# Optimization experiments

Measured on AMD Instinct MI355X. Metric: run time of the kernel, lower is better.

The kernel has to match this reference:

```python
import jax, jax.numpy as jnp
import numpy as np

NUM_EMBEDDINGS = 2048
EMBEDDING_DIM = 512
COMMITMENT_COST = 0.25


def setup_inputs() -> dict:
    key = jax.random.key(0)
    k1, k2 = jax.random.split(key)
    IP_score = jax.random.normal(k1, (256, 51, 512), dtype=jnp.float32)
    emb_weight = jax.random.normal(k2, (NUM_EMBEDDINGS, EMBEDDING_DIM), dtype=jnp.float32)
    return {"IP_score": IP_score, "emb_weight": emb_weight}


def reference(IP_score, emb_weight):
    sg = jax.lax.stop_gradient
    bs, kpts, seq = IP_score.shape
    x = IP_score.reshape(bs, kpts // 3, 3, seq)          # [bs, kpts/3, 3, D]
    flat = x.reshape(-1, seq)                             # [N, D], N = bs*kpts

    # pairwise squared L2 distances to codebook: [N, K]
    d = (jnp.sum(flat * flat, axis=1, keepdims=True)
         + jnp.sum(emb_weight * emb_weight, axis=1)
         - 2.0 * flat @ emb_weight.T)

    # nearest (argmin) and the 3rd-smallest index (coding_idx[:, 2] in torch)
    _, idx3 = jax.lax.top_k(-d, 3)                        # ascending distance order
    nearest = idx3[:, 0]
    third = idx3[:, 2]

    quantized = jnp.take(emb_weight, nearest, axis=0).reshape(x.shape)
    second_quantized = jnp.take(emb_weight, third, axis=0).reshape(x.shape)

    # commitment loss (quantized is detached in the original)
    e_latent_loss = jnp.mean((sg(quantized) - x) ** 2)
    k_loss = COMMITMENT_COST * e_latent_loss

    # straight-through estimator
    quantized_st = x + sg(quantized - x)
    second_st = x + sg(second_quantized - x)

    feature_EMA = quantized_st.reshape(bs, kpts, seq)
    sec_EMA = second_st.reshape(bs, kpts, seq)

    cp_score = 1.0 - (jnp.linalg.norm(feature_EMA - IP_score)
                      / jnp.linalg.norm(sec_EMA - IP_score))
    return (cp_score, k_loss, feature_EMA)
```

## Files before the change

kernel.cpp:

```cpp
#include <hip/hip_runtime.h>
#include <hip/hip_bf16.h>
#include <math.h>

#define RM 13056
#define KD 512
#define NE 2048
#define NELEM 6684672.0

#define BM 128
#define BN 256
#define BK 32
#define NKT (KD / BK)
#define NBLK (NE / BN)
#define NCAND (NBLK * 4)
#define NTAIL (RM / 4)

typedef __attribute__((ext_vector_type(8))) short bf16x8;
typedef __attribute__((ext_vector_type(4))) float f32x4;
typedef unsigned long long ull;

__device__ __forceinline__ void dma16(const void* g, void* l) {
  __builtin_amdgcn_global_load_lds((const __attribute__((address_space(1))) void*)g,
                                   (__attribute__((address_space(3))) void*)l, 16, 0, 0);
}

__device__ __forceinline__ ull packdi(float d, int ix) {
  unsigned u = __float_as_uint(d);
  u ^= (unsigned)((int)u >> 31) | 0x80000000u;
  return ((ull)u << 32) | (unsigned)ix;
}

#define XB (RM * 64 / 256)
#define EB (NE * 64 / 256)
#define NB (NE / 4)
__device__ __forceinline__ void split_chunks(const float* __restrict__ src,
                                             unsigned short* __restrict__ hi,
                                             int rows, int o) {
  int t4 = o >> 2;
  int kt = t4 / rows;
  int row = t4 - kt * rows;
  int slot = o & 3;
  int q = slot ^ ((row >> 1) & 3);
  const float* s = src + (size_t)row * KD + kt * 32 + q * 8;
  float4 v0 = ((const float4*)s)[0];
  float4 v1 = ((const float4*)s)[1];
  float f[8] = {v0.x, v0.y, v0.z, v0.w, v1.x, v1.y, v1.z, v1.w};
  unsigned hh[4];
#pragma unroll
  for (int j = 0; j < 4; ++j) {
    __hip_bfloat16 b0 = __float2bfloat16(f[2 * j]);
    __hip_bfloat16 b1 = __float2bfloat16(f[2 * j + 1]);
    hh[j] = (unsigned)*(unsigned short*)&b0 | ((unsigned)*(unsigned short*)&b1 << 16);
  }
  ((uint4*)hi)[o] = make_uint4(hh[0], hh[1], hh[2], hh[3]);
}

__global__ __launch_bounds__(256) void k_prep(const float* __restrict__ X,
                                              const float* __restrict__ E,
                                              unsigned short* __restrict__ Xh,
                                              unsigned short* __restrict__ Eh,
                                              float* __restrict__ EN) {
  const int b = blockIdx.x, tid = threadIdx.x;
  if (b < XB) {
    split_chunks(X, Xh, RM, b * 256 + tid);
  } else if (b < XB + EB) {
    split_chunks(E, Eh, NE, (b - XB) * 256 + tid);
  } else {
    int n = (b - XB - EB) * 4 + (tid >> 6);
    int lane = tid & 63;
    const float* e = E + (size_t)n * KD;
    float s = 0.f;
#pragma unroll
    for (int j = 0; j < 8; ++j) { float v = e[lane + 64 * j]; s += v * v; }
#pragma unroll
    for (int off = 32; off; off >>= 1) s += __shfl_down(s, off);
    if (lane == 0) EN[n] = s;
  }
}

__device__ __forceinline__ int chidx(int row, int q) {
  return (row * 4 + (q ^ ((row >> 1) & 3))) * 8;
}

__global__ __launch_bounds__(256, 2) void k_dist_bf16(
    const unsigned short* __restrict__ Xh,
    const unsigned short* __restrict__ Eh,
    const float* __restrict__ EN, ull* __restrict__ cand) {
  __shared__ __align__(16) unsigned short sXh[2][BM * BK];
  __shared__ __align__(16) unsigned short sEh[2][BN * BK];
  __shared__ float sEN[BN];

  const int tid = threadIdx.x;
  const int lane = tid & 63;
  const int w = tid >> 6;
  const int quad = lane >> 4;
  const int lx = lane & 15;
  const int rowBase = blockIdx.x * BM;
  const int colBase = blockIdx.y * BN;

  sEN[tid] = EN[colBase + tid];

  int aidx[2], bidx[16];
#pragma unroll
  for (int mt = 0; mt < 2; ++mt) aidx[mt] = chidx(w * 32 + mt * 16 + lx, quad);
#pragma unroll
  for (int ct = 0; ct < 16; ++ct) bidx[ct] = chidx(ct * 16 + lx, quad);

  f32x4 acc[2][16];
#pragma unroll
  for (int mt = 0; mt < 2; ++mt)
#pragma unroll
    for (int ct = 0; ct < 16; ++ct) acc[mt][ct] = (f32x4){0.f, 0.f, 0.f, 0.f};

  for (int kt2 = 0; kt2 < NKT / 2; ++kt2) {
    __syncthreads();
#pragma unroll
    for (int h = 0; h < 2; ++h) {
      const int kt = kt2 * 2 + h;
      const size_t xbase = ((size_t)kt * RM + rowBase) * 4;
      const size_t ebase = ((size_t)kt * NE + colBase) * 4;
#pragma unroll
      for (int i = 0; i < 2; ++i) {
        const int c = i * 256 + tid;
        const int ldsOff = (i * 256 + w * 64) * 8;
        dma16(Xh + (xbase + c) * 8, &sXh[h][ldsOff]);
      }
#pragma unroll
      for (int i = 0; i < 4; ++i) {
        const int c = i * 256 + tid;
        const int ldsOff = (i * 256 + w * 64) * 8;
        dma16(Eh + (ebase + c) * 8, &sEh[h][ldsOff]);
      }
    }
    __syncthreads();

#pragma unroll
    for (int h = 0; h < 2; ++h) {
      bf16x8 Ah[2];
#pragma unroll
      for (int mt = 0; mt < 2; ++mt) Ah[mt] = *(const bf16x8*)&sXh[h][aidx[mt]];
#pragma unroll
      for (int ct = 0; ct < 16; ++ct) {
        bf16x8 Bh = *(const bf16x8*)&sEh[h][bidx[ct]];
#pragma unroll
        for (int mt = 0; mt < 2; ++mt)
          acc[mt][ct] = __builtin_amdgcn_mfma_f32_16x16x32_bf16(Ah[mt], Bh, acc[mt][ct], 0, 0, 0);
      }
    }
  }

  float en[16];
#pragma unroll
  for (int ct = 0; ct < 16; ++ct) en[ct] = sEN[ct * 16 + lx];

#pragma unroll
  for (int mt = 0; mt < 2; ++mt) {
#pragma unroll
    for (int j = 0; j < 4; ++j) {
      float a0 = 3.4e38f, a1 = 3.4e38f, a2 = 3.4e38f, a3 = 3.4e38f;
      int i0 = 0x7fffffff, i1 = i0, i2 = i0, i3 = i0;
#pragma unroll
      for (int ct = 0; ct < 16; ++ct) {
        float d = en[ct] - 2.0f * acc[mt][ct][j];
        int ix = colBase + ct * 16 + lx;
        if (d < a3) {
          if (d < a2) { a3 = a2; i3 = i2;
            if (d < a1) { a2 = a1; i2 = i1;
              if (d < a0) { a1 = a0; i1 = i0; a0 = d; i0 = ix; }
              else { a1 = d; i1 = ix; } }
            else { a2 = d; i2 = ix; } }
          else { a3 = d; i3 = ix; }
        }
      }
      ull k0 = packdi(a0, i0), k1 = packdi(a1, i1);
      ull k2 = packdi(a2, i2), k3 = packdi(a3, i3);
      int pos = 0;
      ull res[4];
#pragma unroll
      for (int r = 0; r < 4; ++r) {
        ull h = pos == 0 ? k0 : pos == 1 ? k1 : pos == 2 ? k2 : pos == 3 ? k3 : ~0ull;
        ull m = h;
#pragma unroll
        for (int step = 1; step < 16; step <<= 1) {
          ull o = __shfl_xor(m, step, 16);
          m = o < m ? o : m;
        }
        res[r] = m;
        pos += (h == m) ? 1 : 0;
      }
      if (lx == 0) {
        int row = rowBase + w * 32 + mt * 16 + quad * 4 + j;
        ull* dst = cand + (size_t)row * NCAND + blockIdx.y * 4;
        dst[0] = res[0]; dst[1] = res[1]; dst[2] = res[2]; dst[3] = res[3];
      }
    }
  }
}

__device__ __forceinline__ void refine_core(const float* __restrict__ X,
                                            const float* __restrict__ E,
                                            const int* ci, int row,
                                            float* __restrict__ outF,
                                            double* __restrict__ part) {
  const int w = threadIdx.x >> 6, lane = threadIdx.x & 63;
  __shared__ double bs1[4], bs3[4];
  const float* xr = X + (size_t)row * KD;
  float4 x0 = *(const float4*)(xr + lane * 8);
  float4 x1 = *(const float4*)(xr + lane * 8 + 4);
  double a[8];
#pragma unroll
  for (int c = 0; c < 8; ++c) {
    const float* er = E + (size_t)ci[c] * KD;
    float4 e0 = *(const float4*)(er + lane * 8);
    float4 e1 = *(const float4*)(er + lane * 8 + 4);
    double s = 0.0;
    double d0 = (double)e0.x - (double)x0.x; s += d0 * d0;
    double d1 = (double)e0.y - (double)x0.y; s += d1 * d1;
    double d2 = (double)e0.z - (double)x0.z; s += d2 * d2;
    double d3 = (double)e0.w - (double)x0.w; s += d3 * d3;
    double d4 = (double)e1.x - (double)x1.x; s += d4 * d4;
    double d5 = (double)e1.y - (double)x1.y; s += d5 * d5;
    double d6 = (double)e1.z - (double)x1.z; s += d6 * d6;
    double d7 = (double)e1.w - (double)x1.w; s += d7 * d7;
    a[c] = s;
  }
#pragma unroll
  for (int c = 0; c < 8; ++c)
#pragma unroll
    for (int off = 32; off; off >>= 1) a[c] += __shfl_down(a[c], off);
  int best = 0;
  if (lane == 0) {
    double d[8]; int id[8];
#pragma unroll
    for (int c = 0; c < 8; ++c) { d[c] = a[c]; id[c] = ci[c]; }
    for (int i = 0; i < 8; ++i)
      for (int j = i + 1; j < 8; ++j)
        if (d[j] < d[i] || (d[j] == d[i] && id[j] < id[i])) {
          double dt = d[i]; d[i] = d[j]; d[j] = dt;
          int it = id[i]; id[i] = id[j]; id[j] = it;
        }
    bs1[w] = d[0];
    bs3[w] = d[2];
    best = id[0];
  }
  best = __shfl(best, 0);
  const float* er = E + (size_t)best * KD;
  *(float4*)(outF + (size_t)row * KD + lane * 8) = *(const float4*)(er + lane * 8);
  *(float4*)(outF + (size_t)row * KD + lane * 8 + 4) = *(const float4*)(er + lane * 8 + 4);
  __syncthreads();
  if (threadIdx.x == 0) {
    part[blockIdx.x * 2] = bs1[0] + bs1[1] + bs1[2] + bs1[3];
    part[blockIdx.x * 2 + 1] = bs3[0] + bs3[1] + bs3[2] + bs3[3];
  }
}

__device__ __forceinline__ ull sort64(ull k, int lane) {
#pragma unroll
  for (int kk = 2; kk <= 64; kk <<= 1) {
#pragma unroll
    for (int j = kk >> 1; j > 0; j >>= 1) {
      ull o = __shfl_xor(k, j, 64);
      bool dirUp = (lane & kk) == 0;
      bool lower = (lane & j) == 0;
      bool pl = o < k;
      bool take = (dirUp == lower) ? pl : !pl;
      if (take) k = o;
    }
  }
  return k;
}

__global__ __launch_bounds__(256) void k_mrf(const float* __restrict__ X,
                                             const float* __restrict__ E,
                                             const ull* __restrict__ cand,
                                             float* __restrict__ outF,
                                             double* __restrict__ part) {
  const int lane = threadIdx.x & 63;
  const int row = blockIdx.x * 4 + (threadIdx.x >> 6);
  ull k = lane < NCAND ? cand[(size_t)row * NCAND + lane] : ~0ull;
  k = sort64(k, lane);
  int ci[8];
#pragma unroll
  for (int c = 0; c < 8; ++c) ci[c] = (int)(__shfl(k, c, 64) & 0xffffffffull);
  refine_core(X, E, ci, row, outF, part);
}

__global__ __launch_bounds__(256) void k_fin(const double* __restrict__ part,
                                             float* __restrict__ out) {
  const int tid = threadIdx.x;
  double a1 = 0.0, a3 = 0.0;
  for (int r = tid; r < NTAIL; r += 256) { a1 += part[2 * r]; a3 += part[2 * r + 1]; }
#pragma unroll
  for (int off = 32; off; off >>= 1) {
    a1 += __shfl_down(a1, off);
    a3 += __shfl_down(a3, off);
  }
  __shared__ double s1[4], s3[4];
  const int w = tid >> 6, lane = tid & 63;
  if (lane == 0) { s1[w] = a1; s3[w] = a3; }
  __syncthreads();
  if (tid == 0) {
    double S1 = s1[0] + s1[1] + s1[2] + s1[3];
    double S3 = s3[0] + s3[1] + s3[2] + s3[3];
    out[0] = (float)(1.0 - sqrt(S1 / S3));
    out[1] = (float)(0.25 * S1 / NELEM);
  }
}

__global__ __launch_bounds__(256) void k_merge(const ull* __restrict__ cand,
                                               int* __restrict__ top8) {
  const int lane = threadIdx.x & 63;
  const int row = blockIdx.x * 4 + (threadIdx.x >> 6);
  ull k = lane < NCAND ? cand[(size_t)row * NCAND + lane] : ~0ull;
  k = sort64(k, lane);
  if (lane < 8) top8[(size_t)row * 8 + lane] = (int)(k & 0xffffffffull);
}

__global__ __launch_bounds__(256) void k_refine_fb(const float* __restrict__ X,
                                                   const float* __restrict__ E,
                                                   const int* __restrict__ top8,
                                                   float* __restrict__ outF,
                                                   double* __restrict__ part) {
  const int row = blockIdx.x * 4 + (threadIdx.x >> 6);
  int ci[8];
#pragma unroll
  for (int c = 0; c < 8; ++c) ci[c] = top8[(size_t)row * 8 + c];
  refine_core(X, E, ci, row, outF, part);
}

extern "C" void kernel_launch(void* const* d_in, const int* in_sizes, int n_in,
                              void* d_out, int out_size, void* d_ws, size_t ws_size,
                              hipStream_t stream) {
  const float* IP = (const float*)d_in[0];
  const float* EMB = (const float*)d_in[1];
  float* out = (float*)d_out;

  char* ws = (char*)d_ws;
  size_t off = 0;
  float* EN = (float*)(ws + off);        off += NE * 4;
  double* part = (double*)(ws + off);    off += (size_t)NTAIL * 2 * 8;
  int* top8 = (int*)(ws + off);          off += (size_t)RM * 8 * 4;
  unsigned short* Xh = (unsigned short*)(ws + off); off += (size_t)RM * KD * 2;
  unsigned short* Ehs = (unsigned short*)(ws + off); off += (size_t)NE * KD * 2;
  ull* candWs = (ull*)(ws + off);        off += (size_t)RM * NCAND * 8;
  const bool fused = ws_size >= off;

  ull* cand = fused ? candWs : (ull*)(out + 2);

  hipLaunchKernelGGL(k_prep, dim3(XB + EB + NB), dim3(256), 0, stream,
                     IP, EMB, Xh, Ehs, EN);
  hipLaunchKernelGGL(k_dist_bf16, dim3(RM / BM, NBLK), dim3(256), 0, stream,
                     Xh, Ehs, EN, cand);
  if (fused) {
    hipLaunchKernelGGL(k_mrf, dim3(NTAIL), dim3(256), 0, stream,
                       IP, EMB, cand, out + 2, part);
  } else {
    hipLaunchKernelGGL(k_merge, dim3(NTAIL), dim3(256), 0, stream, cand, top8);
    hipLaunchKernelGGL(k_refine_fb, dim3(NTAIL), dim3(256), 0, stream,
                       IP, EMB, top8, out + 2, part);
  }
  hipLaunchKernelGGL(k_fin, dim3(1), dim3(256), 0, stream, part, out);
}
```

Baseline: 179.8 us.

## Load bf16 MFMA operands directly from global memory, dropping LDS staging

Removes the LDS double-buffer staging (global_load_lds DMA plus barriers) from the distance GEMM kernel. Each lane now loads its A and B fragments straight from the pre-swizzled global layout into registers every k-step. This cuts the barriers and LDS traffic, but it loses reuse of B tiles across the four waves and of A tiles across the column tiles. The result is more redundant global/L2 reads and register pressure from 16 B vectors held in flight with no prefetch.

Result: slower. 218.7 us (+21.6%).

```diff
diff --git a/kernel.cpp b/kernel.cpp
--- a/kernel.cpp
+++ b/kernel.cpp
@@ -18,11 +18,6 @@
 typedef __attribute__((ext_vector_type(8))) short bf16x8;
 typedef __attribute__((ext_vector_type(4))) float f32x4;
 typedef unsigned long long ull;
-
-__device__ __forceinline__ void dma16(const void* g, void* l) {
-  __builtin_amdgcn_global_load_lds((const __attribute__((address_space(1))) void*)g,
-                                   (__attribute__((address_space(3))) void*)l, 16, 0, 0);
-}
 
 __device__ __forceinline__ ull packdi(float d, int ix) {
   unsigned u = __float_as_uint(d);
@@ -78,16 +73,10 @@
   }
 }
 
-__device__ __forceinline__ int chidx(int row, int q) {
-  return (row * 4 + (q ^ ((row >> 1) & 3))) * 8;
-}
-
 __global__ __launch_bounds__(256, 2) void k_dist_bf16(
     const unsigned short* __restrict__ Xh,
     const unsigned short* __restrict__ Eh,
     const float* __restrict__ EN, ull* __restrict__ cand) {
-  __shared__ __align__(16) unsigned short sXh[2][BM * BK];
-  __shared__ __align__(16) unsigned short sEh[2][BN * BK];
   __shared__ float sEN[BN];
 
   const int tid = threadIdx.x;
@@ -100,11 +89,18 @@
 
   sEN[tid] = EN[colBase + tid];
 
-  int aidx[2], bidx[16];
-#pragma unroll
-  for (int mt = 0; mt < 2; ++mt) aidx[mt] = chidx(w * 32 + mt * 16 + lx, quad);
-#pragma unroll
-  for (int ct = 0; ct < 16; ++ct) bidx[ct] = chidx(ct * 16 + lx, quad);
+  unsigned aoff[2];
+#pragma unroll
+  for (int mt = 0; mt < 2; ++mt) {
+    int row = rowBase + w * 32 + mt * 16 + lx;
+    aoff[mt] = (unsigned)((row * 4 + (quad ^ ((row >> 1) & 3))) * 16);
+  }
+  unsigned boff[16];
+#pragma unroll
+  for (int ct = 0; ct < 16; ++ct) {
+    int n = colBase + ct * 16 + lx;
+    boff[ct] = (unsigned)((n * 4 + (quad ^ ((n >> 1) & 3))) * 16);
+  }
 
   f32x4 acc[2][16];
 #pragma unroll
@@ -112,42 +108,25 @@
 #pragma unroll
     for (int ct = 0; ct < 16; ++ct) acc[mt][ct] = (f32x4){0.f, 0.f, 0.f, 0.f};
 
-  for (int kt2 = 0; kt2 < NKT / 2; ++kt2) {
-    __syncthreads();
-#pragma unroll
-    for (int h = 0; h < 2; ++h) {
-      const int kt = kt2 * 2 + h;
-      const size_t xbase = ((size_t)kt * RM + rowBase) * 4;
-      const size_t ebase = ((size_t)kt * NE + colBase) * 4;
-#pragma unroll
-      for (int i = 0; i < 2; ++i) {
-        const int c = i * 256 + tid;
-        const int ldsOff = (i * 256 + w * 64) * 8;
-        dma16(Xh + (xbase + c) * 8, &sXh[h][ldsOff]);
-      }
-#pragma unroll
-      for (int i = 0; i < 4; ++i) {
-        const int c = i * 256 + tid;
-        const int ldsOff = (i * 256 + w * 64) * 8;
-        dma16(Eh + (ebase + c) * 8, &sEh[h][ldsOff]);
-      }
+  const char* Xp = (const char*)Xh;
+  const char* Ep = (const char*)Eh;
+#pragma unroll 1
+  for (int kt = 0; kt < NKT; ++kt) {
+    bf16x8 A0 = *(const bf16x8*)(Xp + aoff[0]);
+    bf16x8 A1 = *(const bf16x8*)(Xp + aoff[1]);
+    bf16x8 B[16];
+#pragma unroll
+    for (int ct = 0; ct < 16; ++ct) B[ct] = *(const bf16x8*)(Ep + boff[ct]);
+#pragma unroll
+    for (int ct = 0; ct < 16; ++ct) {
+      acc[0][ct] = __builtin_amdgcn_mfma_f32_16x16x32_bf16(A0, B[ct], acc[0][ct], 0, 0, 0);
+      acc[1][ct] = __builtin_amdgcn_mfma_f32_16x16x32_bf16(A1, B[ct], acc[1][ct], 0, 0, 0);
     }
-    __syncthreads();
-
-#pragma unroll
-    for (int h = 0; h < 2; ++h) {
-      bf16x8 Ah[2];
-#pragma unroll
-      for (int mt = 0; mt < 2; ++mt) Ah[mt] = *(const bf16x8*)&sXh[h][aidx[mt]];
-#pragma unroll
-      for (int ct = 0; ct < 16; ++ct) {
-        bf16x8 Bh = *(const bf16x8*)&sEh[h][bidx[ct]];
-#pragma unroll
-        for (int mt = 0; mt < 2; ++mt)
-          acc[mt][ct] = __builtin_amdgcn_mfma_f32_16x16x32_bf16(Ah[mt], Bh, acc[mt][ct], 0, 0, 0);
-      }
-    }
-  }
+    Xp += RM * 64;
+    Ep += NE * 64;
+  }
+
+  __syncthreads();
 
   float en[16];
 #pragma unroll
```
